# Optimization experiments

Measured on AMD Instinct MI355X. Metric: run time of the kernel, lower is better.

The kernel has to match this reference:

```python
import jax, jax.numpy as jnp
import numpy as np

REGION1 = REGION2 = 64
OVERLAP1 = OVERLAP2 = 0
MAX_M1 = MAX_M2 = 16


def dht1(x, axis):
    # 1D discrete Hartley transform along `axis` (real - imag of FFT)
    X = jnp.fft.fft(x, axis=axis)
    return X.real - X.imag


def dht2(x):
    # 2D DHT over last two axes
    X = jnp.fft.fft2(x, axes=(-2, -1))
    return X.real - X.imag


def flip_periodic2(x):
    # Faithful to torch code: flatten last two dims jointly, keep element 0, flip the rest
    s = x.shape
    n = s[-2] * s[-1]
    xf = x.reshape(s[:-2] + (n,))
    zf = jnp.concatenate([xf[..., :1], xf[..., 1:][..., ::-1]], axis=-1)
    return zf.reshape(s)


def hartley_conv2(x, y):
    # x: [b, i, h, w], y: [i, o, h, w] -> [b, o, h, w]; conv via Hartley theorem then idht
    X = dht2(x)
    Y = dht2(y)
    Xf = flip_periodic2(X)
    Yf = flip_periodic2(Y)
    Ye = 0.5 * (Y + Yf)
    Yo = 0.5 * (Y - Yf)
    Z = jnp.einsum('bihw,iohw->bohw', X, Ye) + jnp.einsum('bihw,iohw->bohw', Xf, Yo)
    n = x.shape[-2] * x.shape[-1]
    return dht2(Z) / n  # idht2 (DHT is involutory up to 1/n)


def spectral_conv2d(x, error_np, weights):
    B, Cin, S1, S2 = x.shape
    Cout = weights.shape[1]
    stride1 = REGION1 - OVERLAP1
    stride2 = REGION2 - OVERLAP2
    nr1 = (S1 - OVERLAP1) // stride1 + (1 if (S1 - OVERLAP1) % stride1 else 0)
    nr2 = (S2 - OVERLAP2) // stride2 + (1 if (S2 - OVERLAP2) % stride2 else 0)
    out = jnp.zeros((B, Cout, S1, S2), x.dtype)
    counts = np.zeros((S1, S2), np.float32)
    for i in range(nr1):
        for j in range(nr2):
            s1 = i * stride1; e1 = s1 + REGION1
            if e1 > S1:
                e1 = S1; s1 = max(e1 - REGION1, 0)
            s2 = j * stride2; e2 = s2 + REGION2
            if e2 > S2:
                e2 = S2; s2 = max(e2 - REGION2, 0)
            region_x = x[:, :, s1:e1, s2:e2]
            # adaptive per-sample mode counts from error signal (static, numpy)
            avg = error_np[:, s1:e1, s2:e2].mean(axis=(1, 2))
            mn, mx = avg.min(), avg.max()
            norm = (avg - mn) / (mx - mn) if (mx - mn) > 1e-8 else np.zeros_like(avg)
            nm1 = np.minimum((norm * (MAX_M1 - 1)).astype(np.int64) + 1, MAX_M1)
            nm2 = np.minimum((norm * (MAX_M2 - 1)).astype(np.int64) + 1, MAX_M2)
            # separable per-axis DHT of the region
            region_ht = dht1(dht1(region_x, -2), -1)
            out_ht = jnp.zeros((B, Cout, REGION1, REGION2), x.dtype)
            for b in range(B):
                n1 = int(nm1[b]); n2 = int(nm2[b])
                blk = hartley_conv2(region_ht[b:b + 1, :, :n1, :n2], weights[:, :, :n1, :n2])
                out_ht = out_ht.at[b, :, :n1, :n2].set(blk[0])
            # separable inverse per-axis DHT: dht1 along each axis / region area
            region_out = dht1(dht1(out_ht, -2), -1) / (REGION1 * REGION2)
            out = out.at[:, :, s1:e1, s2:e2].add(region_out)
            counts[s1:e1, s2:e2] += 1
    counts[counts == 0] = 1
    return out / jnp.asarray(counts, x.dtype)


def setup_inputs() -> dict:
    key = jax.random.key(0)
    k1, k2, k3 = jax.random.split(key, 3)
    B, Cin, Cout, S = 8, 32, 32, 256
    scale = 1.0 / (Cin * Cout)
    x = jax.random.normal(k1, (B, Cin, S, S), dtype=jnp.float32)
    error_signal = jax.random.uniform(k2, (B, S, S), dtype=jnp.float32)
    weights = scale * jax.random.uniform(k3, (Cin, Cout, MAX_M1, MAX_M2), dtype=jnp.float32)
    return {"x": x, "error_signal": error_signal, "weights": weights}


def reference(x, error_signal, weights):
    error_np = np.asarray(error_signal)
    return spectral_conv2d(x, error_np, weights)
```

## Files before the change

kernel.cpp:

```cpp
#include <hip/hip_runtime.h>
#include <math.h>

#define NB 8
#define CIN 32
#define COUT 32
#define SS 256
#define REG 64
#define NMAX 16

#define AVG_OFF   0
#define NM_OFF    1024
#define USED_OFF  2048
#define C64_OFF   4096
#define CN_OFF    4352
#define Y_OFF     8192
#define XE_OFF    (8u << 20)
#define XO_OFF    (12u << 20)
#define Z_OFF     (16u << 20)

__global__ void k_tables(float* __restrict__ cyc64, float* __restrict__ cycN) {
    int t = threadIdx.x;
    if (t < 64) {
        double a = (2.0 * M_PI / 64.0) * (double)t;
        cyc64[t] = (float)(cos(a) + sin(a));
    } else if (t < 64 + 136) {
        int e = t - 64;
        int n = 1;
        while (n * (n + 1) / 2 <= e) ++n;
        int j = e - n * (n - 1) / 2;
        double a = (2.0 * M_PI / (double)n) * (double)j;
        cycN[e] = (float)(cos(a) + sin(a));
    }
}

__global__ void k_avg(const float* __restrict__ err, float* __restrict__ avg) {
    int r = blockIdx.x, b = blockIdx.y;
    int ri = r >> 2, rj = r & 3;
    const float* base = err + ((size_t)b * SS + ri * REG) * SS + rj * REG;
    int t = threadIdx.x;
    double s = 0.0;
    for (int it = 0; it < 16; ++it) {
        int u = it * 4 + (t >> 6);
        int v = t & 63;
        s += (double)base[(size_t)u * SS + v];
    }
    __shared__ double sm[256];
    sm[t] = s;
    __syncthreads();
    for (int w = 128; w > 0; w >>= 1) {
        if (t < w) sm[t] += sm[t + w];
        __syncthreads();
    }
    if (t == 0) avg[r * 8 + b] = (float)(sm[0] / 4096.0);
}

__global__ void k_nm(const float* __restrict__ avg, int* __restrict__ nm,
                     int* __restrict__ used) {
    int t = threadIdx.x;
    if (t < 32) used[t] = 0;
    __syncthreads();
    if (t < 16) {
        int r = t;
        float mn = avg[r * 8], mx = mn;
        for (int b = 1; b < NB; ++b) {
            float v = avg[r * 8 + b];
            mn = fminf(mn, v);
            mx = fmaxf(mx, v);
        }
        float d = mx - mn;
        bool ok = ((double)d > 1e-8);
        for (int b = 0; b < NB; ++b) {
            float norm = ok ? (avg[r * 8 + b] - mn) / d : 0.0f;
            float tt = norm * 15.0f;
            int nv = (int)tt + 1;
            if (nv > NMAX) nv = NMAX;
            nm[b * 16 + r] = nv;
            atomicOr(&used[nv], 1);
        }
    }
}

__global__ void k_fwd(const float* __restrict__ x, const int* __restrict__ nm,
                      const float* __restrict__ cyc64, const float* __restrict__ cycN,
                      float* __restrict__ Xe, float* __restrict__ Xo) {
    int i = blockIdx.x, r = blockIdx.y, b = blockIdx.z;
    int n = nm[b * 16 + r];
    int nn = n * n;
    int ri = r >> 2, rj = r & 3;
    int t = threadIdx.x;

    __shared__ __align__(16) float R[64 * 64];
    __shared__ __align__(16) float M1[16 * 68];
    __shared__ float H[256];
    __shared__ float T1[256];
    __shared__ float T2[256];
    __shared__ float cyc64L[64];
    __shared__ float cnL[16];

    if (t < 64) cyc64L[t] = cyc64[t];
    if (t < n)  cnL[t] = cycN[(n * (n - 1)) / 2 + t];

    const float* base = x + (((size_t)(b * CIN + i)) * SS + ri * REG) * SS + rj * REG;
    float4* R4 = (float4*)R;
    {
        int u0 = t >> 4, c4 = t & 15;
        for (int it = 0; it < 4; ++it) {
            int u = it * 16 + u0;
            R4[u * 16 + c4] = *(const float4*)(base + (size_t)u * SS + c4 * 4);
        }
    }
    __syncthreads();

    {
        int p1 = t >> 4, vg = t & 15;
        if (p1 < n) {
            float4 acc = {0.f, 0.f, 0.f, 0.f};
            int idx = 0;
            for (int u = 0; u < 64; ++u) {
                float c = cyc64L[idx]; idx = (idx + p1) & 63;
                float4 rv = R4[u * 16 + vg];
                acc.x += c * rv.x; acc.y += c * rv.y;
                acc.z += c * rv.z; acc.w += c * rv.w;
            }
            *(float4*)&M1[p1 * 68 + vg * 4] = acc;
        }
    }
    __syncthreads();

    int p = 0, q = 0;
    if (t < nn) { p = t / n; q = t - p * n; }

    if (t < nn) {
        float acc = 0.f;
        int idx = 0;
        for (int v = 0; v < 64; ++v) {
            acc += M1[p * 68 + v] * cyc64L[idx];
            idx = (idx + q) & 63;
        }
        H[t] = acc;
    }
    __syncthreads();

    if (t < nn) {
        float acc = 0.f;
        int idx = 0;
        for (int v = 0; v < n; ++v) {
            acc += H[p * n + v] * cnL[idx];
            idx += q; if (idx >= n) idx -= n;
        }
        T1[p * n + q] = acc;
    }
    __syncthreads();
    if (t < nn) {
        float acc = 0.f;
        int idx = 0;
        for (int u = 0; u < n; ++u) {
            acc += T1[u * n + q] * cnL[idx];
            idx += p; if (idx >= n) idx -= n;
        }
        T2[t] = acc;
    }
    __syncthreads();
    if (t < nn) {
        int pf = (p == 0) ? 0 : n - p;
        int qf = (q == 0) ? 0 : n - q;
        H[t] = 0.5f * (T2[p * n + q] + T2[pf * n + q] + T2[p * n + qf] - T2[pf * n + qf]);
    }
    __syncthreads();

    if (t < nn) {
        int fk = (t == 0) ? 0 : nn - t;
        float a = H[t], c = H[fk];
        size_t o = (((size_t)(b * 16 + r)) * CIN + i) * 256 + t;
        Xe[o] = 0.5f * (a + c);
        Xo[o] = 0.5f * (a - c);
    }
}

__global__ void k_wt(const float* __restrict__ wts, const int* __restrict__ used,
                     const float* __restrict__ cycN, float* __restrict__ Y) {
    int n = blockIdx.y + 1;
    if (!used[n]) return;
    int io = blockIdx.x;
    int t = threadIdx.x;
    int nn = n * n;
    __shared__ float Wt[256];
    __shared__ float T1[256];
    __shared__ float T2[256];
    __shared__ float cnL[16];
    Wt[t] = wts[(size_t)io * 256 + t];
    if (t < n) cnL[t] = cycN[(n * (n - 1)) / 2 + t];
    __syncthreads();
    int p = 0, q = 0;
    if (t < nn) { p = t / n; q = t - p * n; }
    if (t < nn) {
        float acc = 0.f;
        int idx = 0;
        for (int v = 0; v < n; ++v) {
            acc += Wt[p * 16 + v] * cnL[idx];
            idx += q; if (idx >= n) idx -= n;
        }
        T1[p * n + q] = acc;
    }
    __syncthreads();
    if (t < nn) {
        float acc = 0.f;
        int idx = 0;
        for (int u = 0; u < n; ++u) {
            acc += T1[u * n + q] * cnL[idx];
            idx += p; if (idx >= n) idx -= n;
        }
        T2[t] = acc;
    }
    __syncthreads();
    if (t < nn) {
        int pf = (p == 0) ? 0 : n - p;
        int qf = (q == 0) ? 0 : n - q;
        float v = 0.5f * (T2[p * n + q] + T2[pf * n + q] + T2[p * n + qf] - T2[pf * n + qf]);
        int m = n - 1;
        int ps2 = m * (m + 1) * (2 * m + 1) / 6;
        Y[(size_t)1024 * ps2 + (size_t)io * nn + t] = v;
    }
}

__global__ void k_z(const float* __restrict__ Xe, const float* __restrict__ Xo,
                    const float* __restrict__ Y, const int* __restrict__ nm,
                    float* __restrict__ Z) {
    int br = blockIdx.y;
    int og = blockIdx.x * 4;
    int b = br >> 4, r = br & 15;
    int n = nm[b * 16 + r];
    int nn = n * n;
    int t = threadIdx.x;
    if (t >= nn) return;
    int m = n - 1;
    int ps2 = m * (m + 1) * (2 * m + 1) / 6;
    const float* Yb = Y + (size_t)1024 * ps2;
    int fk = (t == 0) ? 0 : nn - t;
    float acc[4] = {0.f, 0.f, 0.f, 0.f};
    size_t xbase = (size_t)br * CIN * 256;
    for (int i = 0; i < CIN; ++i) {
        float xe = Xe[xbase + i * 256 + t];
        float xo = Xo[xbase + i * 256 + t];
        const float* yi = Yb + (size_t)(i * COUT + og) * nn;
#pragma unroll
        for (int oo = 0; oo < 4; ++oo) {
            acc[oo] += xe * yi[oo * nn + t] + xo * yi[oo * nn + fk];
        }
    }
    size_t zbase = (size_t)br * COUT * 256;
#pragma unroll
    for (int oo = 0; oo < 4; ++oo) Z[zbase + (og + oo) * 256 + t] = acc[oo];
}

__global__ void k_out(const float* __restrict__ Z, const int* __restrict__ nm,
                      const float* __restrict__ cyc64, const float* __restrict__ cycN,
                      float* __restrict__ out) {
    int o = blockIdx.x, r = blockIdx.y, b = blockIdx.z;
    int n = nm[b * 16 + r];
    int nn = n * n;
    int t = threadIdx.x;
    int br = b * 16 + r;

    __shared__ float Zs[256];
    __shared__ float T1[256];
    __shared__ float T2[256];
    __shared__ float Bk[256];
    __shared__ __align__(16) float E1[16 * 64];
    __shared__ float cyc64L[64];
    __shared__ float cnL[16];

    if (t < 64) cyc64L[t] = cyc64[t];
    if (t < n)  cnL[t] = cycN[(n * (n - 1)) / 2 + t];
    if (t < nn) Zs[t] = Z[((size_t)br * COUT + o) * 256 + t];
    __syncthreads();

    int p = 0, q = 0;
    if (t < nn) { p = t / n; q = t - p * n; }

    if (t < nn) {
        float acc = 0.f;
        int idx = 0;
        for (int v = 0; v < n; ++v) {
            acc += Zs[p * n + v] * cnL[idx];
            idx += q; if (idx >= n) idx -= n;
        }
        T1[p * n + q] = acc;
    }
    __syncthreads();
    if (t < nn) {
        float acc = 0.f;
        int idx = 0;
        for (int u = 0; u < n; ++u) {
            acc += T1[u * n + q] * cnL[idx];
            idx += p; if (idx >= n) idx -= n;
        }
        T2[t] = acc;
    }
    __syncthreads();
    if (t < nn) {
        int pf = (p == 0) ? 0 : n - p;
        int qf = (q == 0) ? 0 : n - q;
        Bk[t] = 0.5f * (T2[p * n + q] + T2[pf * n + q] + T2[p * n + qf] - T2[pf * n + qf])
                / (float)nn;
    }
    __syncthreads();

    for (int mm = t; mm < n * 64; mm += 256) {
        int pp = mm >> 6, v = mm & 63;
        float acc = 0.f;
        int idx = 0;
        for (int qq = 0; qq < n; ++qq) {
            acc += Bk[pp * n + qq] * cyc64L[idx];
            idx = (idx + v) & 63;
        }
        E1[pp * 64 + v] = acc;
    }
    __syncthreads();

    int ri = r >> 2, rj = r & 3;
    float* ob = out + (((size_t)(b * COUT + o)) * SS + ri * REG) * SS + rj * REG;
    const float4* E14 = (const float4*)E1;
    const float inv = 1.0f / 4096.0f;
    int u0 = t >> 4, vg = t & 15;
    for (int it = 0; it < 4; ++it) {
        int u = it * 16 + u0;
        float4 acc = {0.f, 0.f, 0.f, 0.f};
        int idx = 0;
        for (int pp = 0; pp < n; ++pp) {
            float c = cyc64L[idx]; idx = (idx + u) & 63;
            float4 e = E14[pp * 16 + vg];
            acc.x += c * e.x; acc.y += c * e.y;
            acc.z += c * e.z; acc.w += c * e.w;
        }
        acc.x *= inv; acc.y *= inv; acc.z *= inv; acc.w *= inv;
        *(float4*)(ob + (size_t)u * SS + vg * 4) = acc;
    }
}

extern "C" void kernel_launch(void* const* d_in, const int* in_sizes, int n_in,
                              void* d_out, int out_size, void* d_ws, size_t ws_size,
                              hipStream_t stream) {
    const float* x   = (const float*)d_in[0];
    const float* err = (const float*)d_in[1];
    const float* wts = (const float*)d_in[2];
    float* out = (float*)d_out;
    char* ws = (char*)d_ws;

    float* avg   = (float*)(ws + AVG_OFF);
    int*   nm    = (int*)  (ws + NM_OFF);
    int*   used  = (int*)  (ws + USED_OFF);
    float* cyc64 = (float*)(ws + C64_OFF);
    float* cycN  = (float*)(ws + CN_OFF);
    float* Y     = (float*)(ws + Y_OFF);
    float* Xe    = (float*)(ws + XE_OFF);
    float* Xo    = (float*)(ws + XO_OFF);
    float* Z     = (float*)(ws + Z_OFF);

    k_tables<<<1, 256, 0, stream>>>(cyc64, cycN);
    k_avg<<<dim3(16, NB), 256, 0, stream>>>(err, avg);
    k_nm<<<1, 32, 0, stream>>>(avg, nm, used);
    k_fwd<<<dim3(CIN, 16, NB), 256, 0, stream>>>(x, nm, cyc64, cycN, Xe, Xo);
    k_wt<<<dim3(CIN * COUT, NMAX), 256, 0, stream>>>(wts, used, cycN, Y);
    k_z<<<dim3(8, 128), 256, 0, stream>>>(Xe, Xo, Y, nm, Z);
    k_out<<<dim3(COUT, 16, NB), 256, 0, stream>>>(Z, nm, cyc64, cycN, out);
}
```

Before: 179.4 us.

## Merge setup kernels, inline mode-count computation, and rebalance forward/inverse DHT loops

Measured after the change: 182.6 us. About the same (+1.8%).

```diff
diff --git a/kernel.cpp b/kernel.cpp
--- a/kernel.cpp
+++ b/kernel.cpp
@@ -9,8 +9,6 @@
 #define NMAX 16
 
 #define AVG_OFF   0
-#define NM_OFF    1024
-#define USED_OFF  2048
 #define C64_OFF   4096
 #define CN_OFF    4352
 #define Y_OFF     8192
@@ -18,26 +16,42 @@
 #define XO_OFF    (12u << 20)
 #define Z_OFF     (16u << 20)
 
-__global__ void k_tables(float* __restrict__ cyc64, float* __restrict__ cycN) {
-    int t = threadIdx.x;
-    if (t < 64) {
-        double a = (2.0 * M_PI / 64.0) * (double)t;
-        cyc64[t] = (float)(cos(a) + sin(a));
-    } else if (t < 64 + 136) {
-        int e = t - 64;
-        int n = 1;
-        while (n * (n + 1) / 2 <= e) ++n;
-        int j = e - n * (n - 1) / 2;
-        double a = (2.0 * M_PI / (double)n) * (double)j;
-        cycN[e] = (float)(cos(a) + sin(a));
-    }
-}
-
-__global__ void k_avg(const float* __restrict__ err, float* __restrict__ avg) {
+__device__ __forceinline__ int region_n(const float* __restrict__ avg, int r, int b) {
+    float mn = avg[r * 8], mx = mn;
+    for (int bb = 1; bb < NB; ++bb) {
+        float v = avg[r * 8 + bb];
+        mn = fminf(mn, v);
+        mx = fmaxf(mx, v);
+    }
+    float d = mx - mn;
+    bool ok = ((double)d > 1e-8);
+    float norm = ok ? (avg[r * 8 + b] - mn) / d : 0.0f;
+    float tt = norm * 15.0f;
+    int nv = (int)tt + 1;
+    return nv > NMAX ? NMAX : nv;
+}
+
+__global__ void k_avg(const float* __restrict__ err, float* __restrict__ avg,
+                      float* __restrict__ cyc64, float* __restrict__ cycN) {
+    int t = threadIdx.x;
+    if (blockIdx.x == 16) {
+        if (blockIdx.y != 0) return;
+        if (t < 64) {
+            double a = (2.0 * M_PI / 64.0) * (double)t;
+            cyc64[t] = (float)(cos(a) + sin(a));
+        } else if (t < 64 + 136) {
+            int e = t - 64;
+            int n = 1;
+            while (n * (n + 1) / 2 <= e) ++n;
+            int j = e - n * (n - 1) / 2;
+            double a = (2.0 * M_PI / (double)n) * (double)j;
+            cycN[e] = (float)(cos(a) + sin(a));
+        }
+        return;
+    }
     int r = blockIdx.x, b = blockIdx.y;
     int ri = r >> 2, rj = r & 3;
     const float* base = err + ((size_t)b * SS + ri * REG) * SS + rj * REG;
-    int t = threadIdx.x;
     double s = 0.0;
     for (int it = 0; it < 16; ++it) {
         int u = it * 4 + (t >> 6);
@@ -54,37 +68,11 @@
     if (t == 0) avg[r * 8 + b] = (float)(sm[0] / 4096.0);
 }
 
-__global__ void k_nm(const float* __restrict__ avg, int* __restrict__ nm,
-                     int* __restrict__ used) {
-    int t = threadIdx.x;
-    if (t < 32) used[t] = 0;
-    __syncthreads();
-    if (t < 16) {
-        int r = t;
-        float mn = avg[r * 8], mx = mn;
-        for (int b = 1; b < NB; ++b) {
-            float v = avg[r * 8 + b];
-            mn = fminf(mn, v);
-            mx = fmaxf(mx, v);
-        }
-        float d = mx - mn;
-        bool ok = ((double)d > 1e-8);
-        for (int b = 0; b < NB; ++b) {
-            float norm = ok ? (avg[r * 8 + b] - mn) / d : 0.0f;
-            float tt = norm * 15.0f;
-            int nv = (int)tt + 1;
-            if (nv > NMAX) nv = NMAX;
-            nm[b * 16 + r] = nv;
-            atomicOr(&used[nv], 1);
-        }
-    }
-}
-
-__global__ void k_fwd(const float* __restrict__ x, const int* __restrict__ nm,
+__global__ void k_fwd(const float* __restrict__ x, const float* __restrict__ avg,
                       const float* __restrict__ cyc64, const float* __restrict__ cycN,
                       float* __restrict__ Xe, float* __restrict__ Xo) {
     int i = blockIdx.x, r = blockIdx.y, b = blockIdx.z;
-    int n = nm[b * 16 + r];
+    int n = region_n(avg, r, b);
     int nn = n * n;
     int ri = r >> 2, rj = r & 3;
     int t = threadIdx.x;
@@ -112,17 +100,47 @@
     __syncthreads();
 
     {
-        int p1 = t >> 4, vg = t & 15;
-        if (p1 < n) {
-            float4 acc = {0.f, 0.f, 0.f, 0.f};
-            int idx = 0;
-            for (int u = 0; u < 64; ++u) {
-                float c = cyc64L[idx]; idx = (idx + p1) & 63;
-                float4 rv = R4[u * 16 + vg];
-                acc.x += c * rv.x; acc.y += c * rv.y;
-                acc.z += c * rv.z; acc.w += c * rv.w;
-            }
-            *(float4*)&M1[p1 * 68 + vg * 4] = acc;
+        int uq = t >> 6, ps = (t >> 4) & 3, vg = t & 15;
+        int p0 = ps, p1 = ps + 4, p2 = ps + 8, p3 = ps + 12;
+        int i0 = (p0 * (uq << 4)) & 63;
+        int i1 = (p1 * (uq << 4)) & 63;
+        int i2 = (p2 * (uq << 4)) & 63;
+        int i3 = (p3 * (uq << 4)) & 63;
+        float4 a0 = {0.f,0.f,0.f,0.f}, a1 = a0, a2 = a0, a3 = a0;
+        int ubase = (uq << 4) * 16 + vg;
+        for (int uu = 0; uu < 16; ++uu) {
+            float4 rv = R4[ubase + uu * 16];
+            if (p0 < n) { float c = cyc64L[i0];
+                a0.x += c*rv.x; a0.y += c*rv.y; a0.z += c*rv.z; a0.w += c*rv.w; }
+            if (p1 < n) { float c = cyc64L[i1];
+                a1.x += c*rv.x; a1.y += c*rv.y; a1.z += c*rv.z; a1.w += c*rv.w; }
+            if (p2 < n) { float c = cyc64L[i2];
+                a2.x += c*rv.x; a2.y += c*rv.y; a2.z += c*rv.z; a2.w += c*rv.w; }
+            if (p3 < n) { float c = cyc64L[i3];
+                a3.x += c*rv.x; a3.y += c*rv.y; a3.z += c*rv.z; a3.w += c*rv.w; }
+            i0 = (i0 + p0) & 63; i1 = (i1 + p1) & 63;
+            i2 = (i2 + p2) & 63; i3 = (i3 + p3) & 63;
+        }
+        __syncthreads();
+        float4* P4 = R4;
+        int pb = (uq << 8) + vg;
+        if (p0 < n) P4[pb + p0 * 16] = a0;
+        if (p1 < n) P4[pb + p1 * 16] = a1;
+        if (p2 < n) P4[pb + p2 * 16] = a2;
+        if (p3 < n) P4[pb + p3 * 16] = a3;
+        __syncthreads();
+        int pr = t >> 4, vr = t & 15;
+        if (pr < n) {
+            float4 q0 = P4[pr * 16 + vr];
+            float4 q1 = P4[256 + pr * 16 + vr];
+            float4 q2 = P4[512 + pr * 16 + vr];
+            float4 q3 = P4[768 + pr * 16 + vr];
+            float4 s;
+            s.x = (q0.x + q1.x) + (q2.x + q3.x);
+            s.y = (q0.y + q1.y) + (q2.y + q3.y);
+            s.z = (q0.z + q1.z) + (q2.z + q3.z);
+            s.w = (q0.w + q1.w) + (q2.w + q3.w);
+            *(float4*)&M1[pr * 68 + vr * 4] = s;
         }
     }
     __syncthreads();
@@ -177,59 +195,60 @@
     }
 }
 
-__global__ void k_wt(const float* __restrict__ wts, const int* __restrict__ used,
-                     const float* __restrict__ cycN, float* __restrict__ Y) {
-    int n = blockIdx.y + 1;
-    if (!used[n]) return;
+__global__ void k_wt(const float* __restrict__ wts, const float* __restrict__ cycN,
+                     float* __restrict__ Y) {
     int io = blockIdx.x;
     int t = threadIdx.x;
-    int nn = n * n;
     __shared__ float Wt[256];
     __shared__ float T1[256];
     __shared__ float T2[256];
     __shared__ float cnL[16];
     Wt[t] = wts[(size_t)io * 256 + t];
-    if (t < n) cnL[t] = cycN[(n * (n - 1)) / 2 + t];
-    __syncthreads();
-    int p = 0, q = 0;
-    if (t < nn) { p = t / n; q = t - p * n; }
-    if (t < nn) {
-        float acc = 0.f;
-        int idx = 0;
-        for (int v = 0; v < n; ++v) {
-            acc += Wt[p * 16 + v] * cnL[idx];
-            idx += q; if (idx >= n) idx -= n;
-        }
-        T1[p * n + q] = acc;
-    }
-    __syncthreads();
-    if (t < nn) {
-        float acc = 0.f;
-        int idx = 0;
-        for (int u = 0; u < n; ++u) {
-            acc += T1[u * n + q] * cnL[idx];
-            idx += p; if (idx >= n) idx -= n;
-        }
-        T2[t] = acc;
-    }
-    __syncthreads();
-    if (t < nn) {
-        int pf = (p == 0) ? 0 : n - p;
-        int qf = (q == 0) ? 0 : n - q;
-        float v = 0.5f * (T2[p * n + q] + T2[pf * n + q] + T2[p * n + qf] - T2[pf * n + qf]);
-        int m = n - 1;
-        int ps2 = m * (m + 1) * (2 * m + 1) / 6;
-        Y[(size_t)1024 * ps2 + (size_t)io * nn + t] = v;
+    for (int n = 1; n <= NMAX; ++n) {
+        int nn = n * n;
+        __syncthreads();
+        if (t < n) cnL[t] = cycN[(n * (n - 1)) / 2 + t];
+        __syncthreads();
+        int p = 0, q = 0;
+        if (t < nn) { p = t / n; q = t - p * n; }
+        if (t < nn) {
+            float acc = 0.f;
+            int idx = 0;
+            for (int v = 0; v < n; ++v) {
+                acc += Wt[p * 16 + v] * cnL[idx];
+                idx += q; if (idx >= n) idx -= n;
+            }
+            T1[p * n + q] = acc;
+        }
+        __syncthreads();
+        if (t < nn) {
+            float acc = 0.f;
+            int idx = 0;
+            for (int u = 0; u < n; ++u) {
+                acc += T1[u * n + q] * cnL[idx];
+                idx += p; if (idx >= n) idx -= n;
+            }
+            T2[t] = acc;
+        }
+        __syncthreads();
+        if (t < nn) {
+            int pf = (p == 0) ? 0 : n - p;
+            int qf = (q == 0) ? 0 : n - q;
+            float v = 0.5f * (T2[p * n + q] + T2[pf * n + q] + T2[p * n + qf] - T2[pf * n + qf]);
+            int m = n - 1;
+            int ps2 = m * (m + 1) * (2 * m + 1) / 6;
+            Y[(size_t)1024 * ps2 + (size_t)io * nn + t] = v;
+        }
     }
 }
 
 __global__ void k_z(const float* __restrict__ Xe, const float* __restrict__ Xo,
-                    const float* __restrict__ Y, const int* __restrict__ nm,
+                    const float* __restrict__ Y, const float* __restrict__ avg,
                     float* __restrict__ Z) {
     int br = blockIdx.y;
     int og = blockIdx.x * 4;
     int b = br >> 4, r = br & 15;
-    int n = nm[b * 16 + r];
+    int n = region_n(avg, r, b);
     int nn = n * n;
     int t = threadIdx.x;
     if (t >= nn) return;
@@ -239,6 +258,7 @@
     int fk = (t == 0) ? 0 : nn - t;
     float acc[4] = {0.f, 0.f, 0.f, 0.f};
     size_t xbase = (size_t)br * CIN * 256;
+#pragma unroll 2
     for (int i = 0; i < CIN; ++i) {
         float xe = Xe[xbase + i * 256 + t];
         float xo = Xo[xbase + i * 256 + t];
@@ -253,11 +273,11 @@
     for (int oo = 0; oo < 4; ++oo) Z[zbase + (og + oo) * 256 + t] = acc[oo];
 }
 
-__global__ void k_out(const float* __restrict__ Z, const int* __restrict__ nm,
+__global__ void k_out(const float* __restrict__ Z, const float* __restrict__ avg,
                       const float* __restrict__ cyc64, const float* __restrict__ cycN,
                       float* __restrict__ out) {
     int o = blockIdx.x, r = blockIdx.y, b = blockIdx.z;
-    int n = nm[b * 16 + r];
+    int n = region_n(avg, r, b);
     int nn = n * n;
     int t = threadIdx.x;
     int br = b * 16 + r;
@@ -323,19 +343,28 @@
     const float4* E14 = (const float4*)E1;
     const float inv = 1.0f / 4096.0f;
     int u0 = t >> 4, vg = t & 15;
-    for (int it = 0; it < 4; ++it) {
-        int u = it * 16 + u0;
-        float4 acc = {0.f, 0.f, 0.f, 0.f};
-        int idx = 0;
-        for (int pp = 0; pp < n; ++pp) {
-            float c = cyc64L[idx]; idx = (idx + u) & 63;
-            float4 e = E14[pp * 16 + vg];
-            acc.x += c * e.x; acc.y += c * e.y;
-            acc.z += c * e.z; acc.w += c * e.w;
-        }
-        acc.x *= inv; acc.y *= inv; acc.z *= inv; acc.w *= inv;
-        *(float4*)(ob + (size_t)u * SS + vg * 4) = acc;
-    }
+    int uA = u0, uB = 16 + u0, uC = 32 + u0, uD = 48 + u0;
+    int iA = 0, iB = 0, iC = 0, iD = 0;
+    float4 aA = {0.f,0.f,0.f,0.f}, aB = aA, aC = aA, aD = aA;
+    for (int pp = 0; pp < n; ++pp) {
+        float4 e = E14[pp * 16 + vg];
+        float cA = cyc64L[iA]; iA = (iA + uA) & 63;
+        float cB = cyc64L[iB]; iB = (iB + uB) & 63;
+        float cC = cyc64L[iC]; iC = (iC + uC) & 63;
+        float cD = cyc64L[iD]; iD = (iD + uD) & 63;
+        aA.x += cA*e.x; aA.y += cA*e.y; aA.z += cA*e.z; aA.w += cA*e.w;
+        aB.x += cB*e.x; aB.y += cB*e.y; aB.z += cB*e.z; aB.w += cB*e.w;
+        aC.x += cC*e.x; aC.y += cC*e.y; aC.z += cC*e.z; aC.w += cC*e.w;
+        aD.x += cD*e.x; aD.y += cD*e.y; aD.z += cD*e.z; aD.w += cD*e.w;
+    }
+    aA.x *= inv; aA.y *= inv; aA.z *= inv; aA.w *= inv;
+    aB.x *= inv; aB.y *= inv; aB.z *= inv; aB.w *= inv;
+    aC.x *= inv; aC.y *= inv; aC.z *= inv; aC.w *= inv;
+    aD.x *= inv; aD.y *= inv; aD.z *= inv; aD.w *= inv;
+    *(float4*)(ob + (size_t)uA * SS + vg * 4) = aA;
+    *(float4*)(ob + (size_t)uB * SS + vg * 4) = aB;
+    *(float4*)(ob + (size_t)uC * SS + vg * 4) = aC;
+    *(float4*)(ob + (size_t)uD * SS + vg * 4) = aD;
 }
 
 extern "C" void kernel_launch(void* const* d_in, const int* in_sizes, int n_in,
@@ -348,8 +377,6 @@
     char* ws = (char*)d_ws;
 
     float* avg   = (float*)(ws + AVG_OFF);
-    int*   nm    = (int*)  (ws + NM_OFF);
-    int*   used  = (int*)  (ws + USED_OFF);
     float* cyc64 = (float*)(ws + C64_OFF);
     float* cycN  = (float*)(ws + CN_OFF);
     float* Y     = (float*)(ws + Y_OFF);
@@ -357,11 +384,9 @@
     float* Xo    = (float*)(ws + XO_OFF);
     float* Z     = (float*)(ws + Z_OFF);
 
-    k_tables<<<1, 256, 0, stream>>>(cyc64, cycN);
-    k_avg<<<dim3(16, NB), 256, 0, stream>>>(err, avg);
-    k_nm<<<1, 32, 0, stream>>>(avg, nm, used);
-    k_fwd<<<dim3(CIN, 16, NB), 256, 0, stream>>>(x, nm, cyc64, cycN, Xe, Xo);
-    k_wt<<<dim3(CIN * COUT, NMAX), 256, 0, stream>>>(wts, used, cycN, Y);
-    k_z<<<dim3(8, 128), 256, 0, stream>>>(Xe, Xo, Y, nm, Z);
-    k_out<<<dim3(COUT, 16, NB), 256, 0, stream>>>(Z, nm, cyc64, cycN, out);
-}
+    k_avg<<<dim3(17, NB), 256, 0, stream>>>(err, avg, cyc64, cycN);
+    k_wt<<<dim3(CIN * COUT), 256, 0, stream>>>(wts, cycN, Y);
+    k_fwd<<<dim3(CIN, 16, NB), 256, 0, stream>>>(x, avg, cyc64, cycN, Xe, Xo);
+    k_z<<<dim3(8, 128), 256, 0, stream>>>(Xe, Xo, Y, avg, Z);
+    k_out<<<dim3(COUT, 16, NB), 256, 0, stream>>>(Z, avg, cyc64, cycN, out);
+}
```
